# Optimization experiments

Measured on AMD Instinct MI355X. Metric: run time of the kernel, lower is better.

## Reference

```python
import jax, jax.numpy as jnp
import numpy as np

N = 50000
E = 800000
D = 128          # in_channels == hidden_channels
L = 3            # num_layers
JK = D * L       # jk 'cat' output
H2 = D // 2      # classifier hidden
C = 2            # out classes
EPS = 1e-5


def setup_inputs() -> dict:
    key = jax.random.key(0)
    ks = jax.random.split(key, 16)
    x = jax.random.normal(ks[0], (N, D), dtype=jnp.float32)
    edge_index = jax.random.randint(ks[1], (2, E), 0, N, dtype=jnp.int64)
    s = 0.05
    Wl = jax.random.normal(ks[2], (L, D, D), dtype=jnp.float32) * s   # lin_l (on aggregated), has bias
    bl = jax.random.normal(ks[3], (L, D), dtype=jnp.float32) * s
    Wr = jax.random.normal(ks[4], (L, D, D), dtype=jnp.float32) * s   # lin_r (on root), no bias
    gamma = jnp.ones((L, D), dtype=jnp.float32)
    beta = jnp.zeros((L, D), dtype=jnp.float32)
    rmean = jax.random.normal(ks[5], (L, D), dtype=jnp.float32) * s
    rvar = jax.random.uniform(ks[6], (L, D), dtype=jnp.float32, minval=0.5, maxval=1.5)
    Wc1 = jax.random.normal(ks[7], (JK, H2), dtype=jnp.float32) * s
    bc1 = jax.random.normal(ks[8], (H2,), dtype=jnp.float32) * s
    Wc2 = jax.random.normal(ks[9], (H2, C), dtype=jnp.float32) * s
    bc2 = jax.random.normal(ks[10], (C,), dtype=jnp.float32) * s
    return {"x": x, "edge_index": edge_index, "Wl": Wl, "bl": bl, "Wr": Wr,
            "gamma": gamma, "beta": beta, "rmean": rmean, "rvar": rvar,
            "Wc1": Wc1, "bc1": bc1, "Wc2": Wc2, "bc2": bc2}


def reference(x, edge_index, Wl, bl, Wr, gamma, beta, rmean, rvar, Wc1, bc1, Wc2, bc2):
    src, dst = edge_index[0], edge_index[1]
    # node in-degree (for mean aggregation), clamp to avoid div-by-zero
    deg = jax.ops.segment_sum(jnp.ones((E,), dtype=x.dtype), dst, num_segments=N)
    inv_deg = 1.0 / jnp.maximum(deg, 1.0)  # [N]

    h = x
    layer_outputs = []
    for i in range(L):
        # SAGEConv(mean): out = lin_l(mean_{j in N(i)} h_j) + lin_r(h_i)
        agg = jax.ops.segment_sum(h[src], dst, num_segments=N) * inv_deg[:, None]  # [N, D]
        h = agg @ Wl[i] + bl[i] + h @ Wr[i]
        # BatchNorm (eval: running stats), then ReLU; Dropout is identity in eval
        h = (h - rmean[i]) * jax.lax.rsqrt(rvar[i] + EPS) * gamma[i] + beta[i]
        h = jax.nn.relu(h)
        layer_outputs.append(h)

    jk = jnp.concatenate(layer_outputs, axis=-1)  # [N, L*D]
    z = jax.nn.relu(jk @ Wc1 + bc1)
    logits = z @ Wc2 + bc2  # [N, 2]
    return logits
```

## Files before the change

kernel.cpp:

```cpp
#include <hip/hip_runtime.h>
#include <hip/hip_fp16.h>
#include <cstdint>
#include <cstddef>

#define DD 128
#define JKD 384
#define EPSV 1e-5f
#define BSH 7
#define NBMAX 512
#define PCH 8192
#define PTH 1024
#define BCAP 8192

typedef __attribute__((ext_vector_type(8))) short bf16x8;
typedef __attribute__((ext_vector_type(4))) float f32x4;
#define MFMA(a, b, c) __builtin_amdgcn_mfma_f32_16x16x32_bf16(a, b, c, 0, 0, 0)

__device__ inline unsigned short f2bf_rne(float f) {
  unsigned u = __float_as_uint(f);
  unsigned r = u + 0x7fffu + ((u >> 16) & 1u);
  return (unsigned short)(r >> 16);
}

__device__ inline void split8(const float* s, bf16x8& hi, bf16x8& lo) {
#pragma unroll
  for (int j = 0; j < 8; ++j) {
    float f = s[j];
    unsigned short h = f2bf_rne(f);
    float fh = __uint_as_float((unsigned)h << 16);
    hi[j] = (short)h;
    lo[j] = (short)f2bf_rne(f - fh);
  }
}

__device__ inline void h8_to_f8(uint4 raw, float* out) {
  const __half2* hp = reinterpret_cast<const __half2*>(&raw);
#pragma unroll
  for (int j = 0; j < 4; ++j) {
    float2 f = __half22float2(hp[j]);
    out[2 * j] = f.x;
    out[2 * j + 1] = f.y;
  }
}


__global__ void zero_int_kernel(int* __restrict__ p, int n) {
  int i = blockIdx.x * blockDim.x + threadIdx.x;
  if (i < n) p[i] = 0;
}

__global__ __launch_bounds__(PTH) void bucket_hist(const int* __restrict__ dst,
                                                   int* __restrict__ bucket_cnt, int E) {
  __shared__ int h[NBMAX];
  int t = threadIdx.x;
  for (int i = t; i < NBMAX; i += PTH) h[i] = 0;
  __syncthreads();
  int base = blockIdx.x * PCH;
#pragma unroll
  for (int it = 0; it < PCH / PTH; ++it) {
    int e = base + it * PTH + t;
    if (e < E) {
      int d = __builtin_nontemporal_load(dst + e);
      atomicAdd(&h[d >> BSH], 1);
    }
  }
  __syncthreads();
  for (int i = t; i < NBMAX; i += PTH)
    if (h[i]) atomicAdd(&bucket_cnt[i], h[i]);
}

__global__ __launch_bounds__(512) void bucket_scan(const int* __restrict__ bucket_cnt,
                                                   int* __restrict__ bucket_start,
                                                   int* __restrict__ bucket_cursor,
                                                   int* __restrict__ row_start, int N, int E) {
  __shared__ int wsum[8];
  __shared__ int wpref[8];
  int t = threadIdx.x;
  int lane = t & 63, wid = t >> 6;
  int v = bucket_cnt[t];
  int sc = v;
#pragma unroll
  for (int off = 1; off < 64; off <<= 1) {
    int u = __shfl_up(sc, off, 64);
    if (lane >= off) sc += u;
  }
  if (lane == 63) wsum[wid] = sc;
  __syncthreads();
  if (t == 0) {
    int a = 0;
#pragma unroll
    for (int w = 0; w < 8; ++w) { wpref[w] = a; a += wsum[w]; }
  }
  __syncthreads();
  int excl = wpref[wid] + sc - v;
  bucket_start[t] = excl;
  bucket_cursor[t] = excl;
  if (t == 0) row_start[N] = E;
}

__global__ __launch_bounds__(PTH) void partition_kernel(const int* __restrict__ src,
                                                        const int* __restrict__ dst,
                                                        int* bucket_cursor,
                                                        unsigned* __restrict__ packed, int E) {
  __shared__ int h[NBMAX];
  __shared__ int lofs[NBMAX];
  __shared__ int res[NBMAX];
  __shared__ int lcur[NBMAX];
  __shared__ int wsum[4];
  __shared__ int wpref[4];
  __shared__ unsigned stage[PCH];
  int t = threadIdx.x;
  int lane = t & 63;
  int base = blockIdx.x * PCH;

  for (int i = t; i < NBMAX; i += PTH) h[i] = 0;
  __syncthreads();
#pragma unroll
  for (int it = 0; it < PCH / PTH; ++it) {
    int e = base + it * PTH + t;
    if (e < E) {
      int d = __builtin_nontemporal_load(dst + e);
      atomicAdd(&h[d >> BSH], 1);
    }
  }
  __syncthreads();
  int c0 = 0, c1 = 0, s = 0, sc = 0;
  if (t < 256) {
    c0 = h[2 * t];
    c1 = h[2 * t + 1];
    s = c0 + c1;
    sc = s;
#pragma unroll
    for (int off = 1; off < 64; off <<= 1) {
      int u = __shfl_up(sc, off, 64);
      if (lane >= off) sc += u;
    }
    if (lane == 63) wsum[t >> 6] = sc;
  }
  __syncthreads();
  if (t == 0) {
    int a = 0;
#pragma unroll
    for (int w = 0; w < 4; ++w) { wpref[w] = a; a += wsum[w]; }
  }
  __syncthreads();
  if (t < 256) {
    int excl = wpref[t >> 6] + sc - s;
    lofs[2 * t] = excl;
    lofs[2 * t + 1] = excl + c0;
    lcur[2 * t] = excl;
    lcur[2 * t + 1] = excl + c0;
    if (c0 > 0) res[2 * t] = atomicAdd(&bucket_cursor[2 * t], c0);
    if (c1 > 0) res[2 * t + 1] = atomicAdd(&bucket_cursor[2 * t + 1], c1);
  }
  __syncthreads();
#pragma unroll
  for (int it = 0; it < PCH / PTH; ++it) {
    int e = base + it * PTH + t;
    if (e < E) {
      int d = __builtin_nontemporal_load(dst + e);
      int sv = __builtin_nontemporal_load(src + e);
      int pos = atomicAdd(&lcur[d >> BSH], 1);
      stage[pos] = ((unsigned)(d & ((1 << BSH) - 1)) << 16) | (unsigned)(sv & 0xffff);
    }
  }
  __syncthreads();
  int wid = t >> 6;
  for (int b = wid; b < NBMAX; b += PTH / 64) {
    int run = h[b];
    if (run == 0) continue;
    int gbase = res[b], lbase = lofs[b];
    for (int j = lane; j < run; j += 64) packed[gbase + j] = stage[lbase + j];
  }
}

__global__ __launch_bounds__(256) void csr_build(const unsigned* __restrict__ packed,
                                                 const int* __restrict__ bucket_start,
                                                 int* __restrict__ row_start,
                                                 float* __restrict__ inv_deg,
                                                 unsigned short* __restrict__ col, int N) {
  __shared__ int cntA[128];
  __shared__ int lcur[128];
  __shared__ int wsum2[2];
  __shared__ int wpref2[2];
  __shared__ unsigned short stage[BCAP];
  int t = threadIdx.x;
  int b = blockIdx.x;
  int s0 = bucket_start[b], s1 = bucket_start[b + 1];
  int cnt = s1 - s0;
  if (t < 128) cntA[t] = 0;
  __syncthreads();
  for (int i = t; i < cnt; i += 256) {
    unsigned p = packed[s0 + i];
    atomicAdd(&cntA[p >> 16], 1);
  }
  __syncthreads();
  if (t < 128) {
    int lane = t & 63, wid = t >> 6;
    int v = cntA[t];
    int sc = v;
#pragma unroll
    for (int off = 1; off < 64; off <<= 1) {
      int u = __shfl_up(sc, off, 64);
      if (lane >= off) sc += u;
    }
    if (lane == 63) wsum2[wid] = sc;
    __syncthreads();
    if (t == 0) { wpref2[0] = 0; wpref2[1] = wsum2[0]; }
    __syncthreads();
    int excl = wpref2[wid] + sc - v;
    lcur[t] = excl;
    int node = b * 128 + t;
    if (node < N) {
      row_start[node] = s0 + excl;
      inv_deg[node] = 1.0f / fmaxf((float)v, 1.0f);
    }
  } else {
    __syncthreads();
    __syncthreads();
  }
  __syncthreads();
  for (int i = t; i < cnt; i += 256) {
    unsigned p = packed[s0 + i];
    int pos = atomicAdd(&lcur[p >> 16], 1);
    unsigned short us = (unsigned short)(p & 0xffff);
    if (pos < BCAP) stage[pos] = us;
    else col[s0 + pos] = us;
  }
  __syncthreads();
  int lim = min(cnt, BCAP);
  for (int i = t; i < lim; i += 256) col[s0 + i] = stage[i];
}

__global__ __launch_bounds__(256) void to_f16_kernel(const float* __restrict__ in, int ld,
                                                     unsigned short* __restrict__ out, int ldo,
                                                     int nrows) {
  int idx = blockIdx.x * 256 + threadIdx.x;
  int r = idx >> 4, cc = (idx & 15) * 8;
  if (r >= nrows) return;
  const float* p = in + (size_t)r * ld + cc;
  float4 a = *reinterpret_cast<const float4*>(p);
  float4 b = *reinterpret_cast<const float4*>(p + 4);
  __half2 h0 = __floats2half2_rn(a.x, a.y);
  __half2 h1 = __floats2half2_rn(a.z, a.w);
  __half2 h2 = __floats2half2_rn(b.x, b.y);
  __half2 h3 = __floats2half2_rn(b.z, b.w);
  uint4 o;
  o.x = *reinterpret_cast<unsigned*>(&h0);
  o.y = *reinterpret_cast<unsigned*>(&h1);
  o.z = *reinterpret_cast<unsigned*>(&h2);
  o.w = *reinterpret_cast<unsigned*>(&h3);
  *reinterpret_cast<uint4*>(out + (size_t)r * ldo + cc) = o;
}

__global__ __launch_bounds__(256) void prep_layer_w(const float* __restrict__ Wl,
                                                    const float* __restrict__ Wr,
                                                    bf16x8* __restrict__ f) {
  int idx = blockIdx.x * 256 + threadIdx.x;
  int lane = idx & 63;
  int ksnt = (idx >> 6) & 31;
  int mat = (idx >> 11) & 1;
  int layer = idx >> 12;
  int ks = ksnt >> 3, nt = ksnt & 7;
  int nn = nt * 16 + (lane & 15);
  int k0 = ks * 32 + (lane >> 4) * 8;
  const float* W = (mat ? Wr : Wl) + (size_t)layer * DD * DD;
  float v[8];
#pragma unroll
  for (int j = 0; j < 8; ++j) v[j] = W[(size_t)(k0 + j) * DD + nn];
  bf16x8 hi, lo;
  split8(v, hi, lo);
  size_t base = (size_t)((layer * 2 + mat) * 2) * 2048 + (size_t)ksnt * 64 + lane;
  f[base] = hi;
  f[base + 2048] = lo;
}

__global__ __launch_bounds__(256) void prep_cls_w(const float* __restrict__ Wc1,
                                                  bf16x8* __restrict__ f) {
  int idx = blockIdx.x * 256 + threadIdx.x;
  if (idx >= 3072) return;
  int lane = idx & 63;
  int ksnt = idx >> 6;
  int ks = ksnt >> 2, nt = ksnt & 3;
  int nn = nt * 16 + (lane & 15);
  int k0 = ks * 32 + (lane >> 4) * 8;
  float v[8];
#pragma unroll
  for (int j = 0; j < 8; ++j) v[j] = Wc1[(size_t)(k0 + j) * 64 + nn];
  bf16x8 hi, lo;
  split8(v, hi, lo);
  f[idx] = hi;
  f[idx + 3072] = lo;
}

__global__ __launch_bounds__(256) void agg16_kernel(const unsigned short* __restrict__ h16,
                                                    int ldh,
                                                    const int* __restrict__ row_start,
                                                    const unsigned short* __restrict__ col,
                                                    const float* __restrict__ inv_deg,
                                                    unsigned short* __restrict__ agg16, int n) {
  int wib = threadIdx.x >> 6;
  int lane = threadIdx.x & 63;
  int node = blockIdx.x * 4 + wib;
  if (node >= n) return;
  int beg = row_start[node];
  int end = row_start[node + 1];
  int q = lane >> 4, l15 = lane & 15;
  float acc[8];
#pragma unroll
  for (int k = 0; k < 8; ++k) acc[k] = 0.f;

  for (int j0 = beg; j0 < end; j0 += 16) {
    int cnt = end - j0;
    if (cnt > 16) cnt = 16;
    int cidx = (int)col[j0 + min(l15, cnt - 1)];
    uint4 raw[4];
    bool val[4];
#pragma unroll
    for (int k = 0; k < 4; ++k) {
      int e = k * 4 + q;
      int s = __shfl(cidx, e < cnt ? e : 0);
      val[k] = e < cnt;
      if (val[k]) raw[k] = *reinterpret_cast<const uint4*>(h16 + (size_t)s * ldh + l15 * 8);
    }
#pragma unroll
    for (int k = 0; k < 4; ++k) {
      if (val[k]) {
        float f8[8];
        h8_to_f8(raw[k], f8);
#pragma unroll
        for (int c = 0; c < 8; ++c) acc[c] += f8[c];
      }
    }
  }
#pragma unroll
  for (int m = 16; m <= 32; m <<= 1) {
#pragma unroll
    for (int k = 0; k < 8; ++k) acc[k] += __shfl_xor(acc[k], m);
  }
  if (lane < 16) {
    float w = inv_deg[node];
    __half2 h0 = __floats2half2_rn(acc[0] * w, acc[1] * w);
    __half2 h1 = __floats2half2_rn(acc[2] * w, acc[3] * w);
    __half2 h2 = __floats2half2_rn(acc[4] * w, acc[5] * w);
    __half2 h3 = __floats2half2_rn(acc[6] * w, acc[7] * w);
    uint4 o;
    o.x = *reinterpret_cast<unsigned*>(&h0);
    o.y = *reinterpret_cast<unsigned*>(&h1);
    o.z = *reinterpret_cast<unsigned*>(&h2);
    o.w = *reinterpret_cast<unsigned*>(&h3);
    *reinterpret_cast<uint4*>(agg16 + (size_t)node * DD + l15 * 8) = o;
  }
}

__global__ __launch_bounds__(256) void layer_gemm_mfma(
    const unsigned short* __restrict__ hin16, int ldh,
    const unsigned short* __restrict__ agg16,
    const bf16x8* __restrict__ Blh_g, const bf16x8* __restrict__ Bll_g,
    const bf16x8* __restrict__ Brh_g, const bf16x8* __restrict__ Brl_g,
    const float* __restrict__ bl, const float* __restrict__ gamma,
    const float* __restrict__ beta, const float* __restrict__ rmean,
    const float* __restrict__ rvar, unsigned short* __restrict__ out16, int n) {
  int t = threadIdx.x;
  int w = t >> 6, lane = t & 63;
  int lane16 = lane & 15, quad = lane >> 4;
  int row0 = blockIdx.x * 64;
  int m = row0 + w * 16 + lane16;
  bool valid = m < n;
  size_t mrow = (size_t)(valid ? m : 0);
  const unsigned short* ap = agg16 + mrow * DD + quad * 8;
  const unsigned short* hp = hin16 + mrow * (size_t)ldh + quad * 8;

  bf16x8 Ah[4], Al[4], Hh[4], Hl[4];
#pragma unroll
  for (int ks = 0; ks < 4; ++ks) {
    float a8[8], h8[8];
    if (valid) {
      uint4 ra = *reinterpret_cast<const uint4*>(ap + ks * 32);
      uint4 rh = *reinterpret_cast<const uint4*>(hp + ks * 32);
      h8_to_f8(ra, a8);
      h8_to_f8(rh, h8);
    } else {
#pragma unroll
      for (int j = 0; j < 8; ++j) { a8[j] = 0.f; h8[j] = 0.f; }
    }
    split8(a8, Ah[ks], Al[ks]);
    split8(h8, Hh[ks], Hl[ks]);
  }

  f32x4 acc[8];
#pragma unroll
  for (int nt = 0; nt < 8; ++nt) acc[nt] = (f32x4){0.f, 0.f, 0.f, 0.f};

#pragma unroll
  for (int ks = 0; ks < 4; ++ks) {
    int fb = ks * 8 * 64 + lane;
    bf16x8 B0[8], B1[8];
#pragma unroll
    for (int nt = 0; nt < 8; ++nt) B0[nt] = Blh_g[fb + nt * 64];
#pragma unroll
    for (int nt = 0; nt < 8; ++nt) acc[nt] = MFMA(Ah[ks], B0[nt], acc[nt]);
#pragma unroll
    for (int nt = 0; nt < 8; ++nt) B1[nt] = Bll_g[fb + nt * 64];
#pragma unroll
    for (int nt = 0; nt < 8; ++nt) acc[nt] = MFMA(Al[ks], B0[nt], acc[nt]);
#pragma unroll
    for (int nt = 0; nt < 8; ++nt) acc[nt] = MFMA(Ah[ks], B1[nt], acc[nt]);
#pragma unroll
    for (int nt = 0; nt < 8; ++nt) B0[nt] = Brh_g[fb + nt * 64];
#pragma unroll
    for (int nt = 0; nt < 8; ++nt) acc[nt] = MFMA(Hh[ks], B0[nt], acc[nt]);
#pragma unroll
    for (int nt = 0; nt < 8; ++nt) B1[nt] = Brl_g[fb + nt * 64];
#pragma unroll
    for (int nt = 0; nt < 8; ++nt) acc[nt] = MFMA(Hl[ks], B0[nt], acc[nt]);
#pragma unroll
    for (int nt = 0; nt < 8; ++nt) acc[nt] = MFMA(Hh[ks], B1[nt], acc[nt]);
  }

#pragma unroll
  for (int nt = 0; nt < 8; ++nt) {
    int c = nt * 16 + lane16;
    float sc = gamma[c] * rsqrtf(rvar[c] + EPSV);
    float sh = (bl[c] - rmean[c]) * sc + beta[c];
#pragma unroll
    for (int r = 0; r < 4; ++r) {
      int orow = row0 + w * 16 + quad * 4 + r;
      if (orow < n) {
        float v = fmaxf(fmaf(acc[nt][r], sc, sh), 0.f);
        __half hv = __float2half_rn(v);
        out16[(size_t)orow * JKD + c] = *reinterpret_cast<unsigned short*>(&hv);
      }
    }
  }
}

__global__ __launch_bounds__(256) void classifier_mfma(
    const unsigned short* __restrict__ jk16, const bf16x8* __restrict__ Bh_g,
    const bf16x8* __restrict__ Bl_g, const float* __restrict__ bc1,
    const float* __restrict__ Wc2, const float* __restrict__ bc2,
    float* __restrict__ out, int n) {
  __shared__ float sZ[64][65];
  int t = threadIdx.x;
  int w = t >> 6, lane = t & 63;
  int lane16 = lane & 15, quad = lane >> 4;
  int row0 = blockIdx.x * 64;
  int m = row0 + w * 16 + lane16;
  bool valid = m < n;
  const unsigned short* jp = jk16 + (size_t)(valid ? m : 0) * JKD + quad * 8;

  f32x4 acc[4];
#pragma unroll
  for (int nt = 0; nt < 4; ++nt) acc[nt] = (f32x4){0.f, 0.f, 0.f, 0.f};

#pragma unroll
  for (int ks = 0; ks < 12; ++ks) {
    float a8[8];
    if (valid) {
      uint4 raw = *reinterpret_cast<const uint4*>(jp + ks * 32);
      h8_to_f8(raw, a8);
    } else {
#pragma unroll
      for (int j = 0; j < 8; ++j) a8[j] = 0.f;
    }
    bf16x8 Jh, Jl;
    split8(a8, Jh, Jl);
    int fb = ks * 4 * 64 + lane;
    bf16x8 B0[4], B1[4];
#pragma unroll
    for (int nt = 0; nt < 4; ++nt) B0[nt] = Bh_g[fb + nt * 64];
#pragma unroll
    for (int nt = 0; nt < 4; ++nt) acc[nt] = MFMA(Jh, B0[nt], acc[nt]);
#pragma unroll
    for (int nt = 0; nt < 4; ++nt) B1[nt] = Bl_g[fb + nt * 64];
#pragma unroll
    for (int nt = 0; nt < 4; ++nt) acc[nt] = MFMA(Jl, B0[nt], acc[nt]);
#pragma unroll
    for (int nt = 0; nt < 4; ++nt) acc[nt] = MFMA(Jh, B1[nt], acc[nt]);
  }

#pragma unroll
  for (int nt = 0; nt < 4; ++nt) {
    int c = nt * 16 + lane16;
    float b1 = bc1[c];
#pragma unroll
    for (int r = 0; r < 4; ++r)
      sZ[w * 16 + quad * 4 + r][c] = fmaxf(acc[nt][r] + b1, 0.f);
  }
  __syncthreads();

  if (t < 128) {
    int r = t >> 1, j = t & 1;
    int gr = row0 + r;
    if (gr < n) {
      float s = bc2[j];
#pragma unroll
      for (int c = 0; c < 64; ++c) s = fmaf(sZ[r][c], Wc2[c * 2 + j], s);
      out[(size_t)gr * 2 + j] = s;
    }
  }
}


extern "C" void kernel_launch(void* const* d_in, const int* in_sizes, int n_in,
                              void* d_out, int out_size, void* d_ws, size_t ws_size,
                              hipStream_t stream) {
  const float* x = (const float*)d_in[0];
  const int* ei = (const int*)d_in[1];
  const float* Wl = (const float*)d_in[2];
  const float* bl = (const float*)d_in[3];
  const float* Wr = (const float*)d_in[4];
  const float* gamma = (const float*)d_in[5];
  const float* beta = (const float*)d_in[6];
  const float* rmean = (const float*)d_in[7];
  const float* rvar = (const float*)d_in[8];
  const float* Wc1 = (const float*)d_in[9];
  const float* bc1 = (const float*)d_in[10];
  const float* Wc2 = (const float*)d_in[11];
  const float* bc2 = (const float*)d_in[12];
  float* out = (float*)d_out;

  const int N = in_sizes[0] / DD;
  const int E = in_sizes[1] / 2;
  const int* src = ei;
  const int* dst = ei + E;

  auto align = [](size_t v) { return (v + 255) & ~(size_t)255; };
  char* ws = (char*)d_ws;
  size_t off = 0;
  int* row_start = (int*)(ws + off);  off = align(off + sizeof(int) * (size_t)(N + 1));
  unsigned short* col = (unsigned short*)(ws + off); off = align(off + sizeof(short) * (size_t)E);
  float* inv_deg = (float*)(ws + off); off = align(off + sizeof(float) * (size_t)N);
  unsigned* packed = (unsigned*)(ws + off); off = align(off + sizeof(unsigned) * (size_t)E);
  int* bucket_cnt = (int*)(ws + off);    off = align(off + sizeof(int) * NBMAX);
  int* bucket_start = (int*)(ws + off);  off = align(off + sizeof(int) * (NBMAX + 1));
  int* bucket_cursor = (int*)(ws + off); off = align(off + sizeof(int) * NBMAX);
  unsigned short* x16 = (unsigned short*)(ws + off);   off = align(off + sizeof(short) * (size_t)N * DD);
  unsigned short* agg16 = (unsigned short*)(ws + off); off = align(off + sizeof(short) * (size_t)N * DD);
  unsigned short* jk16 = (unsigned short*)(ws + off);  off = align(off + sizeof(short) * (size_t)N * JKD);
  bf16x8* wf = (bf16x8*)(ws + off);  off = align(off + (size_t)16 * 3 * 2 * 2 * 2048);
  bf16x8* wcf = (bf16x8*)(ws + off); off = align(off + (size_t)16 * 2 * 3072);

  const int nbuck = (N + 127) >> BSH;
  const int nChunks = (E + PCH - 1) / PCH;

  zero_int_kernel<<<(NBMAX + 255) / 256, 256, 0, stream>>>(bucket_cnt, NBMAX);
  bucket_hist<<<nChunks, PTH, 0, stream>>>(dst, bucket_cnt, E);
  bucket_scan<<<1, 512, 0, stream>>>(bucket_cnt, bucket_start, bucket_cursor, row_start, N, E);
  partition_kernel<<<nChunks, PTH, 0, stream>>>(src, dst, bucket_cursor, packed, E);
  csr_build<<<nbuck, 256, 0, stream>>>(packed, bucket_start, row_start, inv_deg, col, N);

  prep_layer_w<<<48, 256, 0, stream>>>(Wl, Wr, wf);
  prep_cls_w<<<12, 256, 0, stream>>>(Wc1, wcf);
  to_f16_kernel<<<(N * 16 + 255) / 256, 256, 0, stream>>>(x, DD, x16, DD, N);

  int nTiles = (N + 63) / 64;
  for (int i = 0; i < 3; ++i) {
    const unsigned short* gsrc = (i == 0) ? x16 : (jk16 + (size_t)(i - 1) * DD);
    int ldg = (i == 0) ? DD : JKD;
    agg16_kernel<<<(N + 3) / 4, 256, 0, stream>>>(gsrc, ldg, row_start, col, inv_deg, agg16, N);
    bf16x8* Wlf = wf + (size_t)(i * 2 + 0) * 2 * 2048;
    bf16x8* Wrf = wf + (size_t)(i * 2 + 1) * 2 * 2048;
    layer_gemm_mfma<<<nTiles, 256, 0, stream>>>(
        gsrc, ldg, agg16, Wlf, Wlf + 2048, Wrf, Wrf + 2048,
        bl + (size_t)i * DD, gamma + (size_t)i * DD, beta + (size_t)i * DD,
        rmean + (size_t)i * DD, rvar + (size_t)i * DD, jk16 + (size_t)i * DD, N);
  }
  classifier_mfma<<<nTiles, 256, 0, stream>>>(jk16, wcf, wcf + 3072, bc1, Wc2, bc2, out, N);
}
```

Baseline: 321.9 us.

## Fuse neighbor mean-aggregation into layer GEMM kernel via shared-memory staging

The separate gather/aggregate kernel is removed. Each wave of the layer GEMM kernel now aggregates its own 16 nodes in sequence and stages the fp16 means in LDS, so the intermediate agg buffer is never written to or read back from global memory and one launch per layer is saved. The cost is far less parallelism for the latency-bound gather: one wave per node becomes one wave per 16 nodes, handled serially. The zero-init kernel for the bucket counts is also replaced with hipMemsetAsync.

```diff
diff --git a/kernel.cpp b/kernel.cpp
--- a/kernel.cpp
+++ b/kernel.cpp
@@ -11,6 +11,7 @@
 #define PCH 8192
 #define PTH 1024
 #define BCAP 8192
+#define APAD 136
 
 typedef __attribute__((ext_vector_type(8))) short bf16x8;
 typedef __attribute__((ext_vector_type(4))) float f32x4;
@@ -41,12 +42,6 @@
     out[2 * j] = f.x;
     out[2 * j + 1] = f.y;
   }
-}
-
-
-__global__ void zero_int_kernel(int* __restrict__ p, int n) {
-  int i = blockIdx.x * blockDim.x + threadIdx.x;
-  if (i < n) p[i] = 0;
 }
 
 __global__ __launch_bounds__(PTH) void bucket_hist(const int* __restrict__ dst,
@@ -293,96 +288,94 @@
   f[idx + 3072] = lo;
 }
 
-__global__ __launch_bounds__(256) void agg16_kernel(const unsigned short* __restrict__ h16,
-                                                    int ldh,
-                                                    const int* __restrict__ row_start,
-                                                    const unsigned short* __restrict__ col,
-                                                    const float* __restrict__ inv_deg,
-                                                    unsigned short* __restrict__ agg16, int n) {
-  int wib = threadIdx.x >> 6;
-  int lane = threadIdx.x & 63;
-  int node = blockIdx.x * 4 + wib;
-  if (node >= n) return;
-  int beg = row_start[node];
-  int end = row_start[node + 1];
-  int q = lane >> 4, l15 = lane & 15;
-  float acc[8];
-#pragma unroll
-  for (int k = 0; k < 8; ++k) acc[k] = 0.f;
-
-  for (int j0 = beg; j0 < end; j0 += 16) {
-    int cnt = end - j0;
-    if (cnt > 16) cnt = 16;
-    int cidx = (int)col[j0 + min(l15, cnt - 1)];
-    uint4 raw[4];
-    bool val[4];
-#pragma unroll
-    for (int k = 0; k < 4; ++k) {
-      int e = k * 4 + q;
-      int s = __shfl(cidx, e < cnt ? e : 0);
-      val[k] = e < cnt;
-      if (val[k]) raw[k] = *reinterpret_cast<const uint4*>(h16 + (size_t)s * ldh + l15 * 8);
-    }
-#pragma unroll
-    for (int k = 0; k < 4; ++k) {
-      if (val[k]) {
-        float f8[8];
-        h8_to_f8(raw[k], f8);
-#pragma unroll
-        for (int c = 0; c < 8; ++c) acc[c] += f8[c];
-      }
-    }
-  }
-#pragma unroll
-  for (int m = 16; m <= 32; m <<= 1) {
-#pragma unroll
-    for (int k = 0; k < 8; ++k) acc[k] += __shfl_xor(acc[k], m);
-  }
-  if (lane < 16) {
-    float w = inv_deg[node];
-    __half2 h0 = __floats2half2_rn(acc[0] * w, acc[1] * w);
-    __half2 h1 = __floats2half2_rn(acc[2] * w, acc[3] * w);
-    __half2 h2 = __floats2half2_rn(acc[4] * w, acc[5] * w);
-    __half2 h3 = __floats2half2_rn(acc[6] * w, acc[7] * w);
-    uint4 o;
-    o.x = *reinterpret_cast<unsigned*>(&h0);
-    o.y = *reinterpret_cast<unsigned*>(&h1);
-    o.z = *reinterpret_cast<unsigned*>(&h2);
-    o.w = *reinterpret_cast<unsigned*>(&h3);
-    *reinterpret_cast<uint4*>(agg16 + (size_t)node * DD + l15 * 8) = o;
-  }
-}
-
-__global__ __launch_bounds__(256) void layer_gemm_mfma(
-    const unsigned short* __restrict__ hin16, int ldh,
-    const unsigned short* __restrict__ agg16,
+__global__ __launch_bounds__(256) void layer_fused_mfma(
+    const unsigned short* __restrict__ gsrc, int ldg,
+    const int* __restrict__ row_start, const unsigned short* __restrict__ col,
+    const float* __restrict__ inv_deg,
     const bf16x8* __restrict__ Blh_g, const bf16x8* __restrict__ Bll_g,
     const bf16x8* __restrict__ Brh_g, const bf16x8* __restrict__ Brl_g,
     const float* __restrict__ bl, const float* __restrict__ gamma,
     const float* __restrict__ beta, const float* __restrict__ rmean,
     const float* __restrict__ rvar, unsigned short* __restrict__ out16, int n) {
+  __shared__ unsigned short sA[4][16][APAD];
   int t = threadIdx.x;
   int w = t >> 6, lane = t & 63;
   int lane16 = lane & 15, quad = lane >> 4;
+  int l15 = lane16;
   int row0 = blockIdx.x * 64;
+
+  for (int r16 = 0; r16 < 16; ++r16) {
+    int node = row0 + w * 16 + r16;
+    float acc[8];
+#pragma unroll
+    for (int k = 0; k < 8; ++k) acc[k] = 0.f;
+    if (node < n) {
+      int beg = row_start[node];
+      int end = row_start[node + 1];
+      for (int j0 = beg; j0 < end; j0 += 16) {
+        int cnt = end - j0;
+        if (cnt > 16) cnt = 16;
+        int cidx = (int)col[j0 + min(l15, cnt - 1)];
+        uint4 raw[4];
+        bool val[4];
+#pragma unroll
+        for (int k = 0; k < 4; ++k) {
+          int e = k * 4 + quad;
+          int s = __shfl(cidx, e < cnt ? e : 0);
+          val[k] = e < cnt;
+          if (val[k]) raw[k] = *reinterpret_cast<const uint4*>(gsrc + (size_t)s * ldg + l15 * 8);
+        }
+#pragma unroll
+        for (int k = 0; k < 4; ++k) {
+          if (val[k]) {
+            float f8[8];
+            h8_to_f8(raw[k], f8);
+#pragma unroll
+            for (int c = 0; c < 8; ++c) acc[c] += f8[c];
+          }
+        }
+      }
+#pragma unroll
+      for (int m = 16; m <= 32; m <<= 1) {
+#pragma unroll
+        for (int k = 0; k < 8; ++k) acc[k] += __shfl_xor(acc[k], m);
+      }
+      if (lane < 16) {
+        float iw = inv_deg[node];
+        __half2 h0 = __floats2half2_rn(acc[0] * iw, acc[1] * iw);
+        __half2 h1 = __floats2half2_rn(acc[2] * iw, acc[3] * iw);
+        __half2 h2 = __floats2half2_rn(acc[4] * iw, acc[5] * iw);
+        __half2 h3 = __floats2half2_rn(acc[6] * iw, acc[7] * iw);
+        uint4 o;
+        o.x = *reinterpret_cast<unsigned*>(&h0);
+        o.y = *reinterpret_cast<unsigned*>(&h1);
+        o.z = *reinterpret_cast<unsigned*>(&h2);
+        o.w = *reinterpret_cast<unsigned*>(&h3);
+        *reinterpret_cast<uint4*>(&sA[w][r16][l15 * 8]) = o;
+      }
+    } else if (lane < 16) {
+      uint4 z = {0, 0, 0, 0};
+      *reinterpret_cast<uint4*>(&sA[w][r16][l15 * 8]) = z;
+    }
+  }
+
   int m = row0 + w * 16 + lane16;
   bool valid = m < n;
   size_t mrow = (size_t)(valid ? m : 0);
-  const unsigned short* ap = agg16 + mrow * DD + quad * 8;
-  const unsigned short* hp = hin16 + mrow * (size_t)ldh + quad * 8;
+  const unsigned short* hp = gsrc + mrow * (size_t)ldg + quad * 8;
 
   bf16x8 Ah[4], Al[4], Hh[4], Hl[4];
 #pragma unroll
   for (int ks = 0; ks < 4; ++ks) {
     float a8[8], h8[8];
+    uint4 ra = *reinterpret_cast<const uint4*>(&sA[w][lane16][quad * 8 + ks * 32]);
+    h8_to_f8(ra, a8);
     if (valid) {
-      uint4 ra = *reinterpret_cast<const uint4*>(ap + ks * 32);
       uint4 rh = *reinterpret_cast<const uint4*>(hp + ks * 32);
-      h8_to_f8(ra, a8);
       h8_to_f8(rh, h8);
     } else {
 #pragma unroll
-      for (int j = 0; j < 8; ++j) { a8[j] = 0.f; h8[j] = 0.f; }
+      for (int j = 0; j < 8; ++j) h8[j] = 0.f;
     }
     split8(a8, Ah[ks], Al[ks]);
     split8(h8, Hh[ks], Hl[ks]);
@@ -536,7 +529,6 @@
   int* bucket_start = (int*)(ws + off);  off = align(off + sizeof(int) * (NBMAX + 1));
   int* bucket_cursor = (int*)(ws + off); off = align(off + sizeof(int) * NBMAX);
   unsigned short* x16 = (unsigned short*)(ws + off);   off = align(off + sizeof(short) * (size_t)N * DD);
-  unsigned short* agg16 = (unsigned short*)(ws + off); off = align(off + sizeof(short) * (size_t)N * DD);
   unsigned short* jk16 = (unsigned short*)(ws + off);  off = align(off + sizeof(short) * (size_t)N * JKD);
   bf16x8* wf = (bf16x8*)(ws + off);  off = align(off + (size_t)16 * 3 * 2 * 2 * 2048);
   bf16x8* wcf = (bf16x8*)(ws + off); off = align(off + (size_t)16 * 2 * 3072);
@@ -544,7 +536,7 @@
   const int nbuck = (N + 127) >> BSH;
   const int nChunks = (E + PCH - 1) / PCH;
 
-  zero_int_kernel<<<(NBMAX + 255) / 256, 256, 0, stream>>>(bucket_cnt, NBMAX);
+  hipMemsetAsync(bucket_cnt, 0, sizeof(int) * NBMAX, stream);
   bucket_hist<<<nChunks, PTH, 0, stream>>>(dst, bucket_cnt, E);
   bucket_scan<<<1, 512, 0, stream>>>(bucket_cnt, bucket_start, bucket_cursor, row_start, N, E);
   partition_kernel<<<nChunks, PTH, 0, stream>>>(src, dst, bucket_cursor, packed, E);
@@ -558,11 +550,10 @@
   for (int i = 0; i < 3; ++i) {
     const unsigned short* gsrc = (i == 0) ? x16 : (jk16 + (size_t)(i - 1) * DD);
     int ldg = (i == 0) ? DD : JKD;
-    agg16_kernel<<<(N + 3) / 4, 256, 0, stream>>>(gsrc, ldg, row_start, col, inv_deg, agg16, N);
     bf16x8* Wlf = wf + (size_t)(i * 2 + 0) * 2 * 2048;
     bf16x8* Wrf = wf + (size_t)(i * 2 + 1) * 2 * 2048;
-    layer_gemm_mfma<<<nTiles, 256, 0, stream>>>(
-        gsrc, ldg, agg16, Wlf, Wlf + 2048, Wrf, Wrf + 2048,
+    layer_fused_mfma<<<nTiles, 256, 0, stream>>>(
+        gsrc, ldg, row_start, col, inv_deg, Wlf, Wlf + 2048, Wrf, Wrf + 2048,
         bl + (size_t)i * DD, gamma + (size_t)i * DD, beta + (size_t)i * DD,
         rmean + (size_t)i * DD, rvar + (size_t)i * DD, jk16 + (size_t)i * DD, N);
   }
```

New measurement: 419.9 us. 1.3x slower.
